# Kernel tuning notes

Hardware: AMD Instinct MI355X
Metric: run time of the kernel (lower is better)

Reference implementation:

```python
import jax, jax.numpy as jnp
import numpy as np

KERNEL_MUL = 2.0
KERNEL_NUM = 5


def setup_inputs() -> dict:
    key = jax.random.key(0)
    k1, k2 = jax.random.split(key)
    source = jax.random.normal(k1, (4096, 256), dtype=jnp.float32)
    target = jax.random.normal(k2, (4096, 256), dtype=jnp.float32)
    return {"source": source, "target": target}


def _mmd(source, target):
    n = source.shape[0]
    m = target.shape[0]
    ns = n + m
    total = jnp.concatenate([source, target], axis=0)  # [ns, D]
    # Pairwise squared L2 distances without the O(ns^2 * D) broadcast tensor:
    # ||x_i - x_j||^2 = ||x_i||^2 + ||x_j||^2 - 2 <x_i, x_j>
    sq = jnp.sum(total * total, axis=1)  # [ns]
    l2 = sq[:, None] + sq[None, :] - 2.0 * (total @ total.T)  # [ns, ns]
    # bandwidth computed on detached data in the original (L2_distance.data)
    bandwidth = jax.lax.stop_gradient(jnp.sum(l2)) / (ns * ns - ns)
    bandwidth = bandwidth / (KERNEL_MUL ** (KERNEL_NUM // 2))
    # multi-bandwidth Gaussian kernel sum (fused single pass over l2)
    kernels = jnp.zeros_like(l2)
    for i in range(KERNEL_NUM):
        kernels = kernels + jnp.exp(-l2 / (bandwidth * KERNEL_MUL ** i))
    xx = jnp.sum(kernels[:n, :n]) / (n * n)
    xy = jnp.sum(kernels[:n, n:]) / (-n * m)
    yx = jnp.sum(kernels[n:, :n]) / (-m * n)
    yy = jnp.sum(kernels[n:, n:]) / (m * m)
    return xx + xy + yx + yy


def reference(source, target):
    return _mmd(source, target)
```

## Files before the change

kernel.cpp:

```cpp
#include <hip/hip_runtime.h>
#include <hip/hip_bf16.h>
#include <stdint.h>

#define NS 8192
#define NHALF 4096
#define DIM 256
#define BLK 128
#define BK 32
#define NKT (DIM / BK)
#define NTILES (NS / BLK)
#define HALF_TILES (NHALF / BLK)
#define NTRI (NTILES * (NTILES + 1) / 2)
#define PREP_BLOCKS 256

typedef __attribute__((ext_vector_type(8))) short bf16x8;
typedef __attribute__((ext_vector_type(4))) float f32x4;
typedef __attribute__((ext_vector_type(8))) unsigned short u16x8;

#define XB_OFF   0
#define SQ_OFF   (NS * DIM * 2)
#define PART_OFF (SQ_OFF + NS * 4)
#define ACC_OFF  (PART_OFF + PREP_BLOCKS * DIM * 4)
#define C0_OFF   (ACC_OFF + 8)
#define WS_NEED  (C0_OFF + 16)

__device__ __forceinline__ unsigned short f2bf(float f) {
  unsigned int u = __float_as_uint(f);
  u += 0x7fffu + ((u >> 16) & 1u);
  return (unsigned short)(u >> 16);
}
__device__ __forceinline__ float bf2f(unsigned short h) {
  return __uint_as_float(((unsigned int)h) << 16);
}

__global__ __launch_bounds__(256) void mmd_prep(
    const float* __restrict__ src, const float* __restrict__ tgt,
    unsigned short* __restrict__ Xb, float* __restrict__ sq,
    float* __restrict__ partials) {
  int tid = threadIdx.x;
  int lane32 = tid & 31;
  int rgrp = tid >> 5;
  int c = lane32 * 8;
  int rowBase = blockIdx.x * 32;

  float colpart[8];
#pragma unroll
  for (int j = 0; j < 8; ++j) colpart[j] = 0.f;

#pragma unroll
  for (int p = 0; p < 4; ++p) {
    int row = rowBase + p * 8 + rgrp;
    const float* X = (row < NHALF) ? (src + (size_t)row * DIM)
                                   : (tgt + (size_t)(row - NHALF) * DIM);
    float4 v0 = *(const float4*)(X + c);
    float4 v1 = *(const float4*)(X + c + 4);
    float vals[8] = {v0.x, v0.y, v0.z, v0.w, v1.x, v1.y, v1.z, v1.w};
    u16x8 h;
    float s = 0.f;
#pragma unroll
    for (int j = 0; j < 8; ++j) {
      unsigned short b = f2bf(vals[j]);
      h[j] = b;
      float rb = bf2f(b);
      s += rb * rb;
      colpart[j] += rb;
    }
    *(u16x8*)(Xb + (size_t)row * DIM + c) = h;
    for (int o = 16; o > 0; o >>= 1) s += __shfl_down(s, o, 32);
    if (lane32 == 0) sq[row] = s;
  }

  __shared__ float cp[8][DIM];
  *(float4*)&cp[rgrp][c]     = make_float4(colpart[0], colpart[1], colpart[2], colpart[3]);
  *(float4*)&cp[rgrp][c + 4] = make_float4(colpart[4], colpart[5], colpart[6], colpart[7]);
  __syncthreads();
  float s8 = 0.f;
#pragma unroll
  for (int r = 0; r < 8; ++r) s8 += cp[r][tid];
  partials[blockIdx.x * DIM + tid] = s8;
}

__global__ __launch_bounds__(256) void mmd_band(
    const float* __restrict__ partials, const float* __restrict__ sq,
    float* __restrict__ c0out) {
  __shared__ double buf2[DIM];
  __shared__ float buf1[DIM];
  int tid = threadIdx.x;
  float cs = 0.f;
  for (int b = 0; b < PREP_BLOCKS; ++b) cs += partials[b * DIM + tid];
  float s1 = 0.f;
  for (int k = 0; k < NS / DIM; ++k) s1 += sq[k * DIM + tid];
  buf2[tid] = (double)cs * (double)cs;
  buf1[tid] = s1;
  __syncthreads();
  for (int o = 128; o > 0; o >>= 1) {
    if (tid < o) { buf2[tid] += buf2[tid + o]; buf1[tid] += buf1[tid + o]; }
    __syncthreads();
  }
  if (tid == 0) {
    double S1 = (double)buf1[0];
    double S2 = buf2[0];
    double sum_l2 = 2.0 * (double)NS * S1 - 2.0 * S2;
    double bw = sum_l2 / ((double)NS * (double)NS - (double)NS);
    bw = bw / 4.0;
    c0out[0] = (float)(1.4426950408889634 / bw);
  }
}

#define STAGE(KT, BUF)                                                        \
  {                                                                           \
    _Pragma("unroll") for (int it = 0; it < 2; ++it) {                        \
      int idx = it * 256 + tid;                         \
      int r = idx >> 2, g = idx & 3;          \
      int gs = g ^ ((r >> 1) & 3);          \
      const unsigned short* ga =                                              \
          Xb + (size_t)(rowBase + r) * DIM + (KT)*BK + gs * 8;                \
      __builtin_amdgcn_global_load_lds(                                       \
          (const __attribute__((address_space(1))) void*)ga,                  \
          (__attribute__((address_space(3))) void*)(&As[BUF][idx * 8]), 16,   \
          0, 0);                                                              \
      const unsigned short* gb =                                              \
          Xb + (size_t)(colBase + r) * DIM + (KT)*BK + gs * 8;                \
      __builtin_amdgcn_global_load_lds(                                       \
          (const __attribute__((address_space(1))) void*)gb,                  \
          (__attribute__((address_space(3))) void*)(&Bs[BUF][idx * 8]), 16,   \
          0, 0);                                                              \
    }                                                                         \
  }

__global__ __launch_bounds__(256, 2) void mmd_gram(
    const unsigned short* __restrict__ Xb, const float* __restrict__ sq,
    const float* __restrict__ c0p, double* __restrict__ accK) {
  int l = blockIdx.x;
  int bj = (int)((sqrtf(8.f * (float)l + 1.f) - 1.f) * 0.5f);
  while ((bj + 1) * (bj + 2) / 2 <= l) bj++;
  while (bj * (bj + 1) / 2 > l) bj--;
  int bi = l - bj * (bj + 1) / 2;

  __shared__ __align__(16) unsigned short As[2][BLK * BK];
  __shared__ __align__(16) unsigned short Bs[2][BLK * BK];
  int tid = threadIdx.x;
  int wave = tid >> 6;
  int lane = tid & 63;
  int rowBase = bi * BLK, colBase = bj * BLK;
  int wr = (wave >> 1) * 64;
  int wc = (wave & 1) * 64;

  float c0v = *c0p;
  float sqr[4][4], sqc[4];
  int r4 = (lane >> 4) * 4;
#pragma unroll
  for (int m = 0; m < 4; ++m)
#pragma unroll
    for (int r = 0; r < 4; ++r)
      sqr[m][r] = sq[rowBase + wr + m * 16 + r4 + r];
#pragma unroll
  for (int n = 0; n < 4; ++n)
    sqc[n] = sq[colBase + wc + n * 16 + (lane & 15)];

  f32x4 acc[4][4];
#pragma unroll
  for (int m = 0; m < 4; ++m)
#pragma unroll
    for (int n = 0; n < 4; ++n) acc[m][n] = (f32x4){0.f, 0.f, 0.f, 0.f};

  STAGE(0, 0);
  STAGE(1, 1);

#pragma unroll
  for (int kt = 0; kt < NKT; ++kt) {
    int cur = kt & 1;
    if (kt == NKT - 1)
      asm volatile("s_waitcnt vmcnt(0)" ::: "memory");
    else
      asm volatile("s_waitcnt vmcnt(4)" ::: "memory");
    __builtin_amdgcn_s_barrier();

    bf16x8 af[4], bfr[4];
    int kg = lane >> 4;
#pragma unroll
    for (int m = 0; m < 4; ++m) {
      int r = wr + m * 16 + (lane & 15);
      af[m] = *(const bf16x8*)(&As[cur][r * BK + (kg ^ ((r >> 1) & 3)) * 8]);
    }
#pragma unroll
    for (int n = 0; n < 4; ++n) {
      int r = wc + n * 16 + (lane & 15);
      bfr[n] = *(const bf16x8*)(&Bs[cur][r * BK + (kg ^ ((r >> 1) & 3)) * 8]);
    }
    asm volatile("s_waitcnt lgkmcnt(0)" ::: "memory");
    __builtin_amdgcn_sched_barrier(0);
    __builtin_amdgcn_s_barrier();

    if (kt < NKT - 2) STAGE(kt + 2, cur);

#pragma unroll
    for (int m = 0; m < 4; ++m)
#pragma unroll
      for (int n = 0; n < 4; ++n)
        acc[m][n] = __builtin_amdgcn_mfma_f32_16x16x32_bf16(
            af[m], bfr[n], acc[m][n], 0, 0, 0);
  }

  float cE = -0.0625f * c0v;
  float t2 = -2.f * cE;
  float a_[4][4], b_[4];
#pragma unroll
  for (int m = 0; m < 4; ++m)
#pragma unroll
    for (int r = 0; r < 4; ++r) a_[m][r] = cE * sqr[m][r];
#pragma unroll
  for (int n = 0; n < 4; ++n) b_[n] = cE * sqc[n];

  float tsum = 0.f;
#pragma unroll
  for (int m = 0; m < 4; ++m)
#pragma unroll
    for (int n = 0; n < 4; ++n)
#pragma unroll
      for (int r = 0; r < 4; ++r) {
        float arg = fmaf(acc[m][n][r], t2, a_[m][r] + b_[n]);
        float e4 = exp2f(arg);
        float e3 = e4 * e4;
        float e2 = e3 * e3;
        float e1 = e2 * e2;
        float e0 = e1 * e1;
        tsum += ((e4 + e3) + (e2 + e1)) + e0;
      }

  float* red4 = (float*)&As[0][0];
#pragma unroll
  for (int o = 32; o > 0; o >>= 1) tsum += __shfl_down(tsum, o);
  if (lane == 0) red4[wave] = tsum;
  __syncthreads();
  if (tid == 0) {
    float t = (red4[0] + red4[1]) + (red4[2] + red4[3]);
    float sign = ((bi < HALF_TILES) == (bj < HALF_TILES)) ? 1.f : -1.f;
    float factor = (bi == bj) ? sign : 2.f * sign;
    atomicAdd(accK, (double)(factor * t));
  }
}

__global__ void mmd_final(const double* __restrict__ accK, float* __restrict__ out) {
  out[0] = (float)(accK[0] / ((double)NHALF * (double)NHALF));
}

extern "C" void kernel_launch(void* const* d_in, const int* in_sizes, int n_in,
                              void* d_out, int out_size, void* d_ws, size_t ws_size,
                              hipStream_t stream) {
  if (ws_size < (size_t)WS_NEED) return;
  const float* src = (const float*)d_in[0];
  const float* tgt = (const float*)d_in[1];
  char* ws = (char*)d_ws;
  unsigned short* Xb = (unsigned short*)(ws + XB_OFF);
  float* sq          = (float*)(ws + SQ_OFF);
  float* partials    = (float*)(ws + PART_OFF);
  double* accK       = (double*)(ws + ACC_OFF);
  float* c0          = (float*)(ws + C0_OFF);

  hipMemsetAsync(ws + ACC_OFF, 0, 16, stream);
  mmd_prep<<<PREP_BLOCKS, 256, 0, stream>>>(src, tgt, Xb, sq, partials);
  mmd_band<<<1, 256, 0, stream>>>(partials, sq, c0);
  mmd_gram<<<NTRI, 256, 0, stream>>>(Xb, sq, c0, accK);
  mmd_final<<<1, 1, 0, stream>>>(accK, (float*)d_out);
}
```

Before: 68.22 us.

## Triple-buffer gram LDS, parallelize bandwidth reduction, fold memset into prep

The gram kernel moves from two to three LDS stage buffers, which lets it drop the second barrier per k-step because the prefetch now writes a buffer no wave is reading. The bandwidth kernel now runs 1024 threads, splitting the partials and sq reductions four ways with vectorized loads, to shorten its serial loop. The accumulator memset is replaced by a write inside the prep kernel, removing one launch. Triple buffering raises LDS use per block (from 32 KB to 48 KB), which could limit occupancy.

```diff
diff --git a/kernel.cpp b/kernel.cpp
--- a/kernel.cpp
+++ b/kernel.cpp
@@ -36,8 +36,9 @@
 __global__ __launch_bounds__(256) void mmd_prep(
     const float* __restrict__ src, const float* __restrict__ tgt,
     unsigned short* __restrict__ Xb, float* __restrict__ sq,
-    float* __restrict__ partials) {
+    float* __restrict__ partials, double* __restrict__ accK) {
   int tid = threadIdx.x;
+  if (blockIdx.x == 0 && tid == 0) accK[0] = 0.0;
   int lane32 = tid & 31;
   int rgrp = tid >> 5;
   int c = lane32 * 8;
@@ -80,26 +81,35 @@
   partials[blockIdx.x * DIM + tid] = s8;
 }
 
-__global__ __launch_bounds__(256) void mmd_band(
+__global__ __launch_bounds__(1024) void mmd_band(
     const float* __restrict__ partials, const float* __restrict__ sq,
     float* __restrict__ c0out) {
-  __shared__ double buf2[DIM];
-  __shared__ float buf1[DIM];
+  __shared__ float CS[4][DIM];
+  __shared__ float L1[1024];
+  __shared__ double D2[DIM];
   int tid = threadIdx.x;
+  int q = tid >> 8, col = tid & 255;
   float cs = 0.f;
-  for (int b = 0; b < PREP_BLOCKS; ++b) cs += partials[b * DIM + tid];
-  float s1 = 0.f;
-  for (int k = 0; k < NS / DIM; ++k) s1 += sq[k * DIM + tid];
-  buf2[tid] = (double)cs * (double)cs;
-  buf1[tid] = s1;
+  for (int b = 0; b < PREP_BLOCKS / 4; ++b)
+    cs += partials[(q * 64 + b) * DIM + col];
+  CS[q][col] = cs;
+  const float4* s4 = (const float4*)sq;
+  float4 va = s4[tid * 2], vb = s4[tid * 2 + 1];
+  L1[tid] = (va.x + va.y + va.z + va.w) + (vb.x + vb.y + vb.z + vb.w);
+  __syncthreads();
+  if (tid < DIM) {
+    float ctot = (CS[0][tid] + CS[1][tid]) + (CS[2][tid] + CS[3][tid]);
+    D2[tid] = (double)ctot * (double)ctot;
+    L1[tid] = (L1[tid] + L1[tid + 256]) + (L1[tid + 512] + L1[tid + 768]);
+  }
   __syncthreads();
   for (int o = 128; o > 0; o >>= 1) {
-    if (tid < o) { buf2[tid] += buf2[tid + o]; buf1[tid] += buf1[tid + o]; }
+    if (tid < o) { D2[tid] += D2[tid + o]; L1[tid] += L1[tid + o]; }
     __syncthreads();
   }
   if (tid == 0) {
-    double S1 = (double)buf1[0];
-    double S2 = buf2[0];
+    double S1 = (double)L1[0];
+    double S2 = D2[0];
     double sum_l2 = 2.0 * (double)NS * S1 - 2.0 * S2;
     double bw = sum_l2 / ((double)NS * (double)NS - (double)NS);
     bw = bw / 4.0;
@@ -137,8 +147,8 @@
   while (bj * (bj + 1) / 2 > l) bj--;
   int bi = l - bj * (bj + 1) / 2;
 
-  __shared__ __align__(16) unsigned short As[2][BLK * BK];
-  __shared__ __align__(16) unsigned short Bs[2][BLK * BK];
+  __shared__ __align__(16) unsigned short As[3][BLK * BK];
+  __shared__ __align__(16) unsigned short Bs[3][BLK * BK];
   int tid = threadIdx.x;
   int wave = tid >> 6;
   int lane = tid & 63;
@@ -169,7 +179,7 @@
 
 #pragma unroll
   for (int kt = 0; kt < NKT; ++kt) {
-    int cur = kt & 1;
+    int cur = kt % 3;
     if (kt == NKT - 1)
       asm volatile("s_waitcnt vmcnt(0)" ::: "memory");
     else
@@ -190,9 +200,8 @@
     }
     asm volatile("s_waitcnt lgkmcnt(0)" ::: "memory");
     __builtin_amdgcn_sched_barrier(0);
-    __builtin_amdgcn_s_barrier();
-
-    if (kt < NKT - 2) STAGE(kt + 2, cur);
+
+    if (kt < NKT - 2) STAGE(kt + 2, (kt + 2) % 3);
 
 #pragma unroll
     for (int m = 0; m < 4; ++m)
@@ -258,9 +267,8 @@
   double* accK       = (double*)(ws + ACC_OFF);
   float* c0          = (float*)(ws + C0_OFF);
 
-  hipMemsetAsync(ws + ACC_OFF, 0, 16, stream);
-  mmd_prep<<<PREP_BLOCKS, 256, 0, stream>>>(src, tgt, Xb, sq, partials);
-  mmd_band<<<1, 256, 0, stream>>>(partials, sq, c0);
+  mmd_prep<<<PREP_BLOCKS, 256, 0, stream>>>(src, tgt, Xb, sq, partials, accK);
+  mmd_band<<<1, 1024, 0, stream>>>(partials, sq, c0);
   mmd_gram<<<NTRI, 256, 0, stream>>>(Xb, sq, c0, accK);
   mmd_final<<<1, 1, 0, stream>>>(accK, (float*)d_out);
 }
```

New measurement: 59.06 us. 13.4% less time.
